# Optimization experiments

Measured on AMD Instinct MI355X. Metric: run time of the kernel, lower is better.

The kernel has to match this reference:

```python
import jax, jax.numpy as jnp
import numpy as np

D_MODEL = 1024
NUM_HEADS = 16
D_K = D_MODEL // NUM_HEADS
THETA = 10000.0
BATCH, SEQ = 2, 2048


def _rope(xh, pos):
    # xh: (..., h, s, d_k), pos: (s,) int
    half = D_K // 2
    inv_freq = THETA ** (-jnp.arange(half, dtype=jnp.float32) * 2.0 / D_K)  # (half,)
    ang = pos.astype(jnp.float32)[:, None] * inv_freq[None, :]              # (s, half)
    cos, sin = jnp.cos(ang), jnp.sin(ang)
    x1 = xh[..., 0::2]  # (..., h, s, half)
    x2 = xh[..., 1::2]
    r1 = x1 * cos - x2 * sin
    r2 = x1 * sin + x2 * cos
    out = jnp.stack([r1, r2], axis=-1)            # (..., h, s, half, 2)
    return out.reshape(xh.shape)


def setup_inputs() -> dict:
    key = jax.random.key(0)
    k1, k2, k3 = jax.random.split(key, 3)
    scale_qkv = (6.0 / (3 * D_MODEL + D_MODEL)) ** 0.5  # xavier uniform bound
    scale_o = (6.0 / (2 * D_MODEL)) ** 0.5
    return {
        "x": jax.random.normal(k1, (BATCH, SEQ, D_MODEL), dtype=jnp.float32),
        "token_positions": jnp.arange(SEQ, dtype=jnp.int64 if jax.config.jax_enable_x64 else jnp.int32),
        "qkv_proj": jax.random.uniform(k2, (3 * D_MODEL, D_MODEL), jnp.float32, -scale_qkv, scale_qkv),
        "o_proj": jax.random.uniform(k3, (D_MODEL, D_MODEL), jnp.float32, -scale_o, scale_o),
    }


def reference(x, token_positions, qkv_proj, o_proj):
    # fused QKV projection: x @ qkv_proj^T
    qkv = jnp.einsum('bsd,ed->bse', x, qkv_proj)          # (b, s, 3*d_model)
    q, k, v = jnp.split(qkv, 3, axis=-1)

    def to_heads(t):
        b, s, _ = t.shape
        return t.reshape(b, s, NUM_HEADS, D_K).transpose(0, 2, 1, 3)  # (b, h, s, d_k)

    qh, kh, vh = to_heads(q), to_heads(k), to_heads(v)
    qh = _rope(qh, token_positions)
    kh = _rope(kh, token_positions)

    scores = jnp.einsum('bhqd,bhkd->bhqk', qh, kh) / (D_K ** 0.5)
    s = x.shape[-2]
    causal = jnp.tril(jnp.ones((s, s), dtype=bool))
    scores = jnp.where(causal, scores, -jnp.inf)
    attn = jax.nn.softmax(scores, axis=-1)
    out = jnp.einsum('bhqk,bhkd->bhqd', attn, vh)          # (b, h, s, d_k)
    out = out.transpose(0, 2, 1, 3).reshape(x.shape[0], s, D_MODEL)
    return jnp.einsum('bsd,od->bso', out, o_proj)
```

## Files before the change

### kernel.cpp

```cpp
#include <hip/hip_runtime.h>
#include <hip/hip_bf16.h>
#include <math.h>

typedef __bf16 bf16_t;
typedef __attribute__((ext_vector_type(2))) __bf16 bf16x2;
typedef __attribute__((ext_vector_type(4))) __bf16 bf16x4;
typedef __attribute__((ext_vector_type(8))) __bf16 bf16x8;
typedef __attribute__((ext_vector_type(4))) float f32x4;

#define BATCH  2
#define SEQ    2048
#define DMODEL 1024
#define NHEADS 16
#define DK     64

typedef const __attribute__((address_space(1))) void* gas_t;
typedef __attribute__((address_space(3))) void* las_t;

#define X_N (BATCH * SEQ * DMODEL)
#define W_N (3 * DMODEL * DMODEL)
#define O_N (DMODEL * DMODEL)

__global__ __launch_bounds__(256) void convert_kernel(
    const float* __restrict__ x, const float* __restrict__ w, const float* __restrict__ o,
    bf16_t* __restrict__ xb, bf16_t* __restrict__ wb, bf16_t* __restrict__ ob)
{
    const int gid = blockIdx.x * 256 + threadIdx.x;
    const float* src; bf16_t* dst; int base = gid * 8;
    if (base < X_N)                { src = x; dst = xb; }
    else if (base < X_N + W_N)     { src = w; dst = wb; base -= X_N; }
    else                           { src = o; dst = ob; base -= X_N + W_N; }
    const f32x4 lo = *(const f32x4*)(src + base);
    const f32x4 hi = *(const f32x4*)(src + base + 4);
    bf16x8 r;
    r[0] = (bf16_t)lo[0]; r[1] = (bf16_t)lo[1]; r[2] = (bf16_t)lo[2]; r[3] = (bf16_t)lo[3];
    r[4] = (bf16_t)hi[0]; r[5] = (bf16_t)hi[1]; r[6] = (bf16_t)hi[2]; r[7] = (bf16_t)hi[3];
    *(bf16x8*)(dst + base) = r;
}

__device__ __forceinline__ void gemm128_body(
    const bf16_t* __restrict__ A, const bf16_t* __restrict__ B,
    int rowBase, int colBase, bf16_t* ldsA, bf16_t* ldsB, f32x4 acc[4][4])
{
    const int tid  = threadIdx.x;
    const int lane = tid & 63;
    const int l15  = lane & 15, quad = lane >> 4;
    const int qr   = ((tid >> 6) >> 1) * 64;
    const int qc   = ((tid >> 6) & 1) * 64;

    const int c0 = tid, c1 = tid + 256;
    const int r0 = c0 >> 2, kc0 = (c0 & 3) * 8;
    const int r1 = c1 >> 2, kc1 = (c1 & 3) * 8;
    const bf16_t* ga0 = A + (size_t)(rowBase + r0) * DMODEL + kc0;
    const bf16_t* ga1 = A + (size_t)(rowBase + r1) * DMODEL + kc1;
    const bf16_t* gb0 = B + (size_t)(colBase + r0) * DMODEL + kc0;
    const bf16_t* gb1 = B + (size_t)(colBase + r1) * DMODEL + kc1;

    for (int k0 = 0; k0 < DMODEL; k0 += 32) {
        __syncthreads();
        __builtin_amdgcn_global_load_lds((gas_t)(ga0 + k0), (las_t)(ldsA + c0 * 8), 16, 0, 0);
        __builtin_amdgcn_global_load_lds((gas_t)(ga1 + k0), (las_t)(ldsA + c1 * 8), 16, 0, 0);
        __builtin_amdgcn_global_load_lds((gas_t)(gb0 + k0), (las_t)(ldsB + c0 * 8), 16, 0, 0);
        __builtin_amdgcn_global_load_lds((gas_t)(gb1 + k0), (las_t)(ldsB + c1 * 8), 16, 0, 0);
        __syncthreads();

        bf16x8 af[4], bfr[4];
#pragma unroll
        for (int i = 0; i < 4; ++i)
            af[i] = *(const bf16x8*)&ldsA[(qr + i * 16 + l15) * 32 + quad * 8];
#pragma unroll
        for (int j = 0; j < 4; ++j)
            bfr[j] = *(const bf16x8*)&ldsB[(qc + j * 16 + l15) * 32 + quad * 8];
#pragma unroll
        for (int i = 0; i < 4; ++i)
#pragma unroll
            for (int j = 0; j < 4; ++j)
                acc[i][j] = __builtin_amdgcn_mfma_f32_16x16x32_bf16(af[i], bfr[j], acc[i][j], 0, 0, 0);
    }
}

__global__ __launch_bounds__(256) void qkv_gemm_kernel(
    const bf16_t* __restrict__ x, const bf16_t* __restrict__ w,
    const int* __restrict__ pos,
    bf16_t* __restrict__ qo, bf16_t* __restrict__ ko, bf16_t* __restrict__ vt)
{
    __shared__ bf16_t ldsA[128 * 32];
    __shared__ bf16_t ldsB[128 * 32];
    const int rowBase = blockIdx.y * 128;
    const int colBase = blockIdx.x * 128;
    f32x4 acc[4][4] = {};
    gemm128_body(x, w, rowBase, colBase, ldsA, ldsB, acc);

    const int lane = threadIdx.x & 63;
    const int l15 = lane & 15, quad = lane >> 4;
    const int qr = ((threadIdx.x >> 6) >> 1) * 64;
    const int qc = ((threadIdx.x >> 6) & 1) * 64;
#pragma unroll
    for (int j = 0; j < 4; ++j) {
        const int col  = colBase + qc + j * 16 + l15;
        const int part = col >> 10;
        const int h    = (col & 1023) >> 6;
        const int d    = col & 63;
        bf16_t* op = (part == 0) ? qo : (part == 1) ? ko : vt;
        if (part < 2) {
            const float invf  = exp2f(-(float)(d >> 1) * 0.4152410118609203f);
            const float psign = (d & 1) ? 1.f : -1.f;
#pragma unroll
            for (int i = 0; i < 4; ++i) {
#pragma unroll
                for (int r = 0; r < 4; ++r) {
                    const int m = rowBase + qr + i * 16 + quad * 4 + r;
                    const int b = m >> 11;
                    const int s = m & (SEQ - 1);
                    const float ang = (float)pos[s] * invf;
                    const float sn_ = __sinf(ang);
                    const float c_  = __cosf(ang);
                    const float v = acc[i][j][r];
                    const float p = __shfl_xor(v, 1);
                    const float res = fmaf(p, psign * sn_, v * c_);
                    op[((size_t)(b * NHEADS + h) * SEQ + s) * DK + d] = (bf16_t)res;
                }
            }
        } else {
#pragma unroll
            for (int i = 0; i < 4; ++i) {
#pragma unroll
                for (int r = 0; r < 4; ++r) {
                    const int m = rowBase + qr + i * 16 + quad * 4 + r;
                    const int b = m >> 11;
                    const int s = m & (SEQ - 1);
                    const int sp = (s & ~63) | ((s & 15) << 2) | ((s >> 4) & 3);
                    op[(size_t)(b * NHEADS + h) * SEQ * DK + (size_t)d * SEQ + sp]
                        = (bf16_t)acc[i][j][r];
                }
            }
        }
    }
}

__global__ __launch_bounds__(256) void out_gemm_kernel(
    const bf16_t* __restrict__ a, const bf16_t* __restrict__ w, float* __restrict__ out)
{
    __shared__ bf16_t ldsA[128 * 32];
    __shared__ bf16_t ldsB[64 * 32];
    const int tid  = threadIdx.x;
    const int lane = tid & 63;
    const int l15  = lane & 15, quad = lane >> 4;
    const int wv   = tid >> 6;
    const int rowBase = blockIdx.y * 128;
    const int colBase = blockIdx.x * 64;

    const int c0 = tid, c1 = tid + 256;
    const bf16_t* ga0 = a + (size_t)(rowBase + (c0 >> 2)) * DMODEL + (c0 & 3) * 8;
    const bf16_t* ga1 = a + (size_t)(rowBase + (c1 >> 2)) * DMODEL + (c1 & 3) * 8;
    const bf16_t* gb0 = w + (size_t)(colBase + (tid >> 2)) * DMODEL + (tid & 3) * 8;

    f32x4 acc[2][4] = {};
    for (int k0 = 0; k0 < DMODEL; k0 += 32) {
        __syncthreads();
        __builtin_amdgcn_global_load_lds((gas_t)(ga0 + k0), (las_t)(ldsA + c0 * 8), 16, 0, 0);
        __builtin_amdgcn_global_load_lds((gas_t)(ga1 + k0), (las_t)(ldsA + c1 * 8), 16, 0, 0);
        __builtin_amdgcn_global_load_lds((gas_t)(gb0 + k0), (las_t)(ldsB + tid * 8), 16, 0, 0);
        __syncthreads();

        bf16x8 af[2], bfr[4];
#pragma unroll
        for (int i = 0; i < 2; ++i)
            af[i] = *(const bf16x8*)&ldsA[(wv * 32 + i * 16 + l15) * 32 + quad * 8];
#pragma unroll
        for (int j = 0; j < 4; ++j)
            bfr[j] = *(const bf16x8*)&ldsB[(j * 16 + l15) * 32 + quad * 8];
#pragma unroll
        for (int i = 0; i < 2; ++i)
#pragma unroll
            for (int j = 0; j < 4; ++j)
                acc[i][j] = __builtin_amdgcn_mfma_f32_16x16x32_bf16(af[i], bfr[j], acc[i][j], 0, 0, 0);
    }
#pragma unroll
    for (int i = 0; i < 2; ++i) {
#pragma unroll
        for (int r = 0; r < 4; ++r) {
            const int m = rowBase + wv * 32 + i * 16 + quad * 4 + r;
#pragma unroll
            for (int j = 0; j < 4; ++j)
                out[(size_t)m * DMODEL + colBase + j * 16 + l15] = acc[i][j][r];
        }
    }
}

__global__ __launch_bounds__(512) void attn_kernel(
    const bf16_t* __restrict__ Q, const bf16_t* __restrict__ K,
    const bf16_t* __restrict__ VT, bf16_t* __restrict__ AO)
{
    __shared__ bf16_t Kb[2][64 * 64];
    __shared__ bf16_t Vb[2][64 * 64];
    __shared__ bf16_t Pb[8][16 * 72];

    const int bh = blockIdx.x & 31;
    const int j  = blockIdx.x >> 5;
    const int qb = (j < 8) ? j : 23 - j;
    const int nt = 2 * qb + 2;

    const int tid  = threadIdx.x;
    const int wave = tid >> 6, lane = tid & 63;
    const int l15  = lane & 15, quad = lane >> 4;
    const int q0   = qb * 128 + wave * 16;
    const size_t hb = (size_t)bh * SEQ * DK;

    const int sr = tid >> 3;
    const int sc = ((tid & 7) ^ (sr & 7)) * 8;
    const int dd = tid * 8;

    bf16x8 aq0, aq1;
    {
        const bf16_t* qrow = Q + hb + (size_t)(q0 + l15) * DK + quad * 8;
        aq0 = *(const bf16x8*)qrow;
        aq1 = *(const bf16x8*)(qrow + 32);
#pragma unroll
        for (int i = 0; i < 8; ++i) {
            aq0[i] = (bf16_t)((float)aq0[i] * 0.125f);
            aq1[i] = (bf16_t)((float)aq1[i] * 0.125f);
        }
    }

    f32x4 oacc[4] = {};
    float lsum[4] = {};

    __builtin_amdgcn_global_load_lds((gas_t)(K  + hb + (size_t)sr * DK + sc),
                                     (las_t)(&Kb[0][dd]), 16, 0, 0);
    __builtin_amdgcn_global_load_lds((gas_t)(VT + hb + (size_t)sr * SEQ + sc),
                                     (las_t)(&Vb[0][dd]), 16, 0, 0);
    __syncthreads();

    const int swA = (quad ^ (l15 & 7)) * 8;
    const int swB = ((4 + quad) ^ (l15 & 7)) * 8;

    int buf = 0;
    for (int kb = 0; kb < nt; ++kb) {
        if (kb + 1 < nt) {
            const bf16_t* kg = K  + hb + (size_t)(kb + 1) * 64 * DK;
            const bf16_t* vg = VT + hb + (kb + 1) * 64;
            __builtin_amdgcn_global_load_lds((gas_t)(kg + (size_t)sr * DK + sc),
                                             (las_t)(&Kb[buf ^ 1][dd]), 16, 0, 0);
            __builtin_amdgcn_global_load_lds((gas_t)(vg + (size_t)sr * SEQ + sc),
                                             (las_t)(&Vb[buf ^ 1][dd]), 16, 0, 0);
        }

        const bool act = (kb * 64 <= q0 + 15);
        const bool nm  = (kb * 64 + 63 > q0);

        if (act) {
            bf16x8 kf0[4], kf1[4];
#pragma unroll
            for (int c = 0; c < 4; ++c) {
                kf0[c] = *(const bf16x8*)&Kb[buf][(c * 16 + l15) * 64 + swA];
                kf1[c] = *(const bf16x8*)&Kb[buf][(c * 16 + l15) * 64 + swB];
            }
            f32x4 sc4[4];
#pragma unroll
            for (int c = 0; c < 4; ++c) {
                f32x4 z = {};
                z = __builtin_amdgcn_mfma_f32_16x16x32_bf16(aq0, kf0[c], z, 0, 0, 0);
                z = __builtin_amdgcn_mfma_f32_16x16x32_bf16(aq1, kf1[c], z, 0, 0, 0);
                sc4[c] = z;
            }
#pragma unroll
            for (int r = 0; r < 4; ++r) {
                bf16x4 pr;
#pragma unroll
                for (int c = 0; c < 4; ++c) {
                    float s = sc4[c][r];
                    if (nm) {
                        const int key = kb * 64 + c * 16 + l15;
                        const int qa  = q0 + quad * 4 + r;
                        s = (key <= qa) ? s : -INFINITY;
                    }
                    const float p = __expf(s - 8.0f);
                    lsum[r] += p;
                    pr[c] = (bf16_t)p;
                }
                *(bf16x4*)&Pb[wave][(quad * 4 + r) * 72 + l15 * 4] = pr;
            }
            asm volatile("s_waitcnt lgkmcnt(0)" ::: "memory");

            const bf16x8 ap0 = *(const bf16x8*)&Pb[wave][l15 * 72 + quad * 8];
            const bf16x8 ap1 = *(const bf16x8*)&Pb[wave][l15 * 72 + 32 + quad * 8];
#pragma unroll
            for (int t = 0; t < 4; ++t) {
                const bf16x8 bv0 = *(const bf16x8*)&Vb[buf][(t * 16 + l15) * 64 + swA];
                const bf16x8 bv1 = *(const bf16x8*)&Vb[buf][(t * 16 + l15) * 64 + swB];
                oacc[t] = __builtin_amdgcn_mfma_f32_16x16x32_bf16(ap0, bv0, oacc[t], 0, 0, 0);
                oacc[t] = __builtin_amdgcn_mfma_f32_16x16x32_bf16(ap1, bv1, oacc[t], 0, 0, 0);
            }
        }

        __syncthreads();
        buf ^= 1;
    }

    const int b = bh >> 4, h = bh & 15;
    float inv[4];
#pragma unroll
    for (int r = 0; r < 4; ++r) {
        float s = lsum[r];
        s += __shfl_xor(s, 1);
        s += __shfl_xor(s, 2);
        s += __shfl_xor(s, 4);
        s += __shfl_xor(s, 8);
        inv[r] = 1.0f / s;
    }
#pragma unroll
    for (int t = 0; t < 4; ++t)
#pragma unroll
        for (int r = 0; r < 4; ++r) {
            const int qa = q0 + quad * 4 + r;
            AO[(size_t)(b * SEQ + qa) * DMODEL + h * 64 + t * 16 + l15] =
                (bf16_t)(oacc[t][r] * inv[r]);
        }
}

extern "C" void kernel_launch(void* const* d_in, const int* in_sizes, int n_in,
                              void* d_out, int out_size, void* d_ws, size_t ws_size,
                              hipStream_t stream) {
    (void)in_sizes; (void)n_in; (void)out_size; (void)ws_size;
    const float* x    = (const float*)d_in[0];
    const int*   pos  = (const int*)d_in[1];
    const float* qkvw = (const float*)d_in[2];
    const float* ow   = (const float*)d_in[3];
    float* out = (float*)d_out;

    const size_t HEAD_ELEMS = (size_t)BATCH * NHEADS * SEQ * DK;
    bf16_t* Qw  = (bf16_t*)d_ws;
    bf16_t* Kw  = Qw + HEAD_ELEMS;
    bf16_t* Vt  = Kw + HEAD_ELEMS;
    bf16_t* AO  = Vt + HEAD_ELEMS;
    bf16_t* xb  = AO;
    bf16_t* wb  = AO + X_N;
    bf16_t* ob  = wb + W_N;

    convert_kernel<<<dim3(4096), 256, 0, stream>>>(x, qkvw, ow, xb, wb, ob);
    qkv_gemm_kernel<<<dim3(24, 32), 256, 0, stream>>>(xb, wb, pos, Qw, Kw, Vt);
    attn_kernel<<<dim3(512), 512, 0, stream>>>(Qw, Kw, Vt, AO);
    out_gemm_kernel<<<dim3(16, 32), 256, 0, stream>>>(AO, ob, out);
}
```

Measured before the change: 193.8 us.

## Double GEMM K-tile to 64 with XOR-swizzled LDS and precompute RoPE table

Both projection GEMMs now stage 64-wide K tiles in LDS instead of 32, which halves the number of barrier pairs per output tile. The LDS rows use an XOR swizzle on 16-byte chunks to avoid bank conflicts on the wider rows. The RoPE cos/sin values are computed once per (position, frequency) pair by extra blocks in the convert kernel and stored in a workspace table, so the QKV epilogue no longer evaluates sin/cos per element. The cost is double the LDS footprint, which may reduce occupancy, plus extra global reads of the table in the epilogue.

```diff
diff --git a/kernel.cpp b/kernel.cpp
--- a/kernel.cpp
+++ b/kernel.cpp
@@ -7,6 +7,7 @@
 typedef __attribute__((ext_vector_type(4))) __bf16 bf16x4;
 typedef __attribute__((ext_vector_type(8))) __bf16 bf16x8;
 typedef __attribute__((ext_vector_type(4))) float f32x4;
+typedef __attribute__((ext_vector_type(2))) float f32x2;
 
 #define BATCH  2
 #define SEQ    2048
@@ -20,11 +21,22 @@
 #define X_N (BATCH * SEQ * DMODEL)
 #define W_N (3 * DMODEL * DMODEL)
 #define O_N (DMODEL * DMODEL)
+#define TBL_N (SEQ * 32)
 
 __global__ __launch_bounds__(256) void convert_kernel(
     const float* __restrict__ x, const float* __restrict__ w, const float* __restrict__ o,
-    bf16_t* __restrict__ xb, bf16_t* __restrict__ wb, bf16_t* __restrict__ ob)
-{
+    const int* __restrict__ pos,
+    bf16_t* __restrict__ xb, bf16_t* __restrict__ wb, bf16_t* __restrict__ ob,
+    f32x2* __restrict__ tbl)
+{
+    if (blockIdx.x >= 4096) {
+        const int e  = (blockIdx.x - 4096) * 256 + threadIdx.x;
+        const int s  = e >> 5;
+        const int dp = e & 31;
+        const float ang = (float)pos[s] * exp2f(-(float)dp * 0.4152410118609203f);
+        tbl[e] = (f32x2){ __cosf(ang), __sinf(ang) };
+        return;
+    }
     const int gid = blockIdx.x * 256 + threadIdx.x;
     const float* src; bf16_t* dst; int base = gid * 8;
     if (base < X_N)                { src = x; dst = xb; }
@@ -45,47 +57,53 @@
     const int tid  = threadIdx.x;
     const int lane = tid & 63;
     const int l15  = lane & 15, quad = lane >> 4;
+    const int l7   = l15 & 7;
     const int qr   = ((tid >> 6) >> 1) * 64;
     const int qc   = ((tid >> 6) & 1) * 64;
 
-    const int c0 = tid, c1 = tid + 256;
-    const int r0 = c0 >> 2, kc0 = (c0 & 3) * 8;
-    const int r1 = c1 >> 2, kc1 = (c1 & 3) * 8;
-    const bf16_t* ga0 = A + (size_t)(rowBase + r0) * DMODEL + kc0;
-    const bf16_t* ga1 = A + (size_t)(rowBase + r1) * DMODEL + kc1;
-    const bf16_t* gb0 = B + (size_t)(colBase + r0) * DMODEL + kc0;
-    const bf16_t* gb1 = B + (size_t)(colBase + r1) * DMODEL + kc1;
-
-    for (int k0 = 0; k0 < DMODEL; k0 += 32) {
-        __syncthreads();
-        __builtin_amdgcn_global_load_lds((gas_t)(ga0 + k0), (las_t)(ldsA + c0 * 8), 16, 0, 0);
-        __builtin_amdgcn_global_load_lds((gas_t)(ga1 + k0), (las_t)(ldsA + c1 * 8), 16, 0, 0);
-        __builtin_amdgcn_global_load_lds((gas_t)(gb0 + k0), (las_t)(ldsB + c0 * 8), 16, 0, 0);
-        __builtin_amdgcn_global_load_lds((gas_t)(gb1 + k0), (las_t)(ldsB + c1 * 8), 16, 0, 0);
-        __syncthreads();
-
-        bf16x8 af[4], bfr[4];
-#pragma unroll
-        for (int i = 0; i < 4; ++i)
-            af[i] = *(const bf16x8*)&ldsA[(qr + i * 16 + l15) * 32 + quad * 8];
-#pragma unroll
-        for (int j = 0; j < 4; ++j)
-            bfr[j] = *(const bf16x8*)&ldsB[(qc + j * 16 + l15) * 32 + quad * 8];
-#pragma unroll
-        for (int i = 0; i < 4; ++i)
+    const int sr   = tid >> 3;
+    const int scol = ((tid & 7) ^ (sr & 7)) * 8;
+    const bf16_t* ga = A + (size_t)(rowBase + sr) * DMODEL + scol;
+    const bf16_t* gb = B + (size_t)(colBase + sr) * DMODEL + scol;
+    const int dd = tid * 8;
+
+    for (int k0 = 0; k0 < DMODEL; k0 += 64) {
+        __syncthreads();
+#pragma unroll
+        for (int u = 0; u < 4; ++u) {
+            __builtin_amdgcn_global_load_lds((gas_t)(ga + k0 + (size_t)u * 32 * DMODEL),
+                                             (las_t)(ldsA + dd + u * 2048), 16, 0, 0);
+            __builtin_amdgcn_global_load_lds((gas_t)(gb + k0 + (size_t)u * 32 * DMODEL),
+                                             (las_t)(ldsB + dd + u * 2048), 16, 0, 0);
+        }
+        __syncthreads();
+
+#pragma unroll
+        for (int kk = 0; kk < 2; ++kk) {
+            const int sw = ((kk * 4 + quad) ^ l7) * 8;
+            bf16x8 af[4], bfr[4];
+#pragma unroll
+            for (int i = 0; i < 4; ++i)
+                af[i] = *(const bf16x8*)&ldsA[(qr + i * 16 + l15) * 64 + sw];
 #pragma unroll
             for (int j = 0; j < 4; ++j)
-                acc[i][j] = __builtin_amdgcn_mfma_f32_16x16x32_bf16(af[i], bfr[j], acc[i][j], 0, 0, 0);
+                bfr[j] = *(const bf16x8*)&ldsB[(qc + j * 16 + l15) * 64 + sw];
+#pragma unroll
+            for (int i = 0; i < 4; ++i)
+#pragma unroll
+                for (int j = 0; j < 4; ++j)
+                    acc[i][j] = __builtin_amdgcn_mfma_f32_16x16x32_bf16(af[i], bfr[j], acc[i][j], 0, 0, 0);
+        }
     }
 }
 
 __global__ __launch_bounds__(256) void qkv_gemm_kernel(
     const bf16_t* __restrict__ x, const bf16_t* __restrict__ w,
-    const int* __restrict__ pos,
+    const f32x2* __restrict__ tbl,
     bf16_t* __restrict__ qo, bf16_t* __restrict__ ko, bf16_t* __restrict__ vt)
 {
-    __shared__ bf16_t ldsA[128 * 32];
-    __shared__ bf16_t ldsB[128 * 32];
+    __shared__ bf16_t ldsA[128 * 64];
+    __shared__ bf16_t ldsB[128 * 64];
     const int rowBase = blockIdx.y * 128;
     const int colBase = blockIdx.x * 128;
     f32x4 acc[4][4] = {};
@@ -103,8 +121,8 @@
         const int d    = col & 63;
         bf16_t* op = (part == 0) ? qo : (part == 1) ? ko : vt;
         if (part < 2) {
-            const float invf  = exp2f(-(float)(d >> 1) * 0.4152410118609203f);
             const float psign = (d & 1) ? 1.f : -1.f;
+            const f32x2* trow = tbl + (d >> 1);
 #pragma unroll
             for (int i = 0; i < 4; ++i) {
 #pragma unroll
@@ -112,12 +130,10 @@
                     const int m = rowBase + qr + i * 16 + quad * 4 + r;
                     const int b = m >> 11;
                     const int s = m & (SEQ - 1);
-                    const float ang = (float)pos[s] * invf;
-                    const float sn_ = __sinf(ang);
-                    const float c_  = __cosf(ang);
+                    const f32x2 cs = trow[s * 32];
                     const float v = acc[i][j][r];
                     const float p = __shfl_xor(v, 1);
-                    const float res = fmaf(p, psign * sn_, v * c_);
+                    const float res = fmaf(p, psign * cs[1], v * cs[0]);
                     op[((size_t)(b * NHEADS + h) * SEQ + s) * DK + d] = (bf16_t)res;
                 }
             }
@@ -141,40 +157,51 @@
 __global__ __launch_bounds__(256) void out_gemm_kernel(
     const bf16_t* __restrict__ a, const bf16_t* __restrict__ w, float* __restrict__ out)
 {
-    __shared__ bf16_t ldsA[128 * 32];
-    __shared__ bf16_t ldsB[64 * 32];
+    __shared__ bf16_t ldsA[128 * 64];
+    __shared__ bf16_t ldsB[64 * 64];
     const int tid  = threadIdx.x;
     const int lane = tid & 63;
     const int l15  = lane & 15, quad = lane >> 4;
+    const int l7   = l15 & 7;
     const int wv   = tid >> 6;
     const int rowBase = blockIdx.y * 128;
     const int colBase = blockIdx.x * 64;
 
-    const int c0 = tid, c1 = tid + 256;
-    const bf16_t* ga0 = a + (size_t)(rowBase + (c0 >> 2)) * DMODEL + (c0 & 3) * 8;
-    const bf16_t* ga1 = a + (size_t)(rowBase + (c1 >> 2)) * DMODEL + (c1 & 3) * 8;
-    const bf16_t* gb0 = w + (size_t)(colBase + (tid >> 2)) * DMODEL + (tid & 3) * 8;
+    const int sr   = tid >> 3;
+    const int scol = ((tid & 7) ^ (sr & 7)) * 8;
+    const bf16_t* ga = a + (size_t)(rowBase + sr) * DMODEL + scol;
+    const bf16_t* gb = w + (size_t)(colBase + sr) * DMODEL + scol;
+    const int dd = tid * 8;
 
     f32x4 acc[2][4] = {};
-    for (int k0 = 0; k0 < DMODEL; k0 += 32) {
-        __syncthreads();
-        __builtin_amdgcn_global_load_lds((gas_t)(ga0 + k0), (las_t)(ldsA + c0 * 8), 16, 0, 0);
-        __builtin_amdgcn_global_load_lds((gas_t)(ga1 + k0), (las_t)(ldsA + c1 * 8), 16, 0, 0);
-        __builtin_amdgcn_global_load_lds((gas_t)(gb0 + k0), (las_t)(ldsB + tid * 8), 16, 0, 0);
-        __syncthreads();
-
-        bf16x8 af[2], bfr[4];
-#pragma unroll
-        for (int i = 0; i < 2; ++i)
-            af[i] = *(const bf16x8*)&ldsA[(wv * 32 + i * 16 + l15) * 32 + quad * 8];
-#pragma unroll
-        for (int j = 0; j < 4; ++j)
-            bfr[j] = *(const bf16x8*)&ldsB[(j * 16 + l15) * 32 + quad * 8];
-#pragma unroll
-        for (int i = 0; i < 2; ++i)
+    for (int k0 = 0; k0 < DMODEL; k0 += 64) {
+        __syncthreads();
+#pragma unroll
+        for (int u = 0; u < 4; ++u)
+            __builtin_amdgcn_global_load_lds((gas_t)(ga + k0 + (size_t)u * 32 * DMODEL),
+                                             (las_t)(ldsA + dd + u * 2048), 16, 0, 0);
+#pragma unroll
+        for (int u = 0; u < 2; ++u)
+            __builtin_amdgcn_global_load_lds((gas_t)(gb + k0 + (size_t)u * 32 * DMODEL),
+                                             (las_t)(ldsB + dd + u * 2048), 16, 0, 0);
+        __syncthreads();
+
+#pragma unroll
+        for (int kk = 0; kk < 2; ++kk) {
+            const int sw = ((kk * 4 + quad) ^ l7) * 8;
+            bf16x8 af[2], bfr[4];
+#pragma unroll
+            for (int i = 0; i < 2; ++i)
+                af[i] = *(const bf16x8*)&ldsA[(wv * 32 + i * 16 + l15) * 64 + sw];
 #pragma unroll
             for (int j = 0; j < 4; ++j)
-                acc[i][j] = __builtin_amdgcn_mfma_f32_16x16x32_bf16(af[i], bfr[j], acc[i][j], 0, 0, 0);
+                bfr[j] = *(const bf16x8*)&ldsB[(j * 16 + l15) * 64 + sw];
+#pragma unroll
+            for (int i = 0; i < 2; ++i)
+#pragma unroll
+                for (int j = 0; j < 4; ++j)
+                    acc[i][j] = __builtin_amdgcn_mfma_f32_16x16x32_bf16(af[i], bfr[j], acc[i][j], 0, 0, 0);
+        }
     }
 #pragma unroll
     for (int i = 0; i < 2; ++i) {
@@ -337,9 +364,10 @@
     bf16_t* xb  = AO;
     bf16_t* wb  = AO + X_N;
     bf16_t* ob  = wb + W_N;
-
-    convert_kernel<<<dim3(4096), 256, 0, stream>>>(x, qkvw, ow, xb, wb, ob);
-    qkv_gemm_kernel<<<dim3(24, 32), 256, 0, stream>>>(xb, wb, pos, Qw, Kw, Vt);
+    f32x2*  tbl = (f32x2*)(ob + O_N);
+
+    convert_kernel<<<dim3(4096 + 256), 256, 0, stream>>>(x, qkvw, ow, pos, xb, wb, ob, tbl);
+    qkv_gemm_kernel<<<dim3(24, 32), 256, 0, stream>>>(xb, wb, tbl, Qw, Kw, Vt);
     attn_kernel<<<dim3(512), 512, 0, stream>>>(Qw, Kw, Vt, AO);
     out_gemm_kernel<<<dim3(16, 32), 256, 0, stream>>>(AO, ob, out);
 }
```

Measured after the change: 184.5 us. 4.8% less time.

## Double-buffer out-projection GEMM with BK=64 and XOR-swizzled LDS layout

Applied to the files above, without the earlier changes.

The output-projection GEMM now uses two LDS buffers, prefetching the next 64-wide K slice while MFMAs run on the current one. The K step doubles from 32 to 64, and a XOR swizzle on the column chunk index is meant to avoid LDS bank conflicts on fragment reads. Together these halve the barriers per K and hide global load latency, at the cost of four times the LDS per block, which may reduce occupancy.

```diff
diff --git a/kernel.cpp b/kernel.cpp
--- a/kernel.cpp
+++ b/kernel.cpp
@@ -141,40 +141,66 @@
 __global__ __launch_bounds__(256) void out_gemm_kernel(
     const bf16_t* __restrict__ a, const bf16_t* __restrict__ w, float* __restrict__ out)
 {
-    __shared__ bf16_t ldsA[128 * 32];
-    __shared__ bf16_t ldsB[64 * 32];
+    __shared__ bf16_t ldsA[2 * 128 * 64];
+    __shared__ bf16_t ldsB[2 * 64 * 64];
     const int tid  = threadIdx.x;
     const int lane = tid & 63;
     const int l15  = lane & 15, quad = lane >> 4;
+    const int l7   = l15 & 7;
     const int wv   = tid >> 6;
     const int rowBase = blockIdx.y * 128;
     const int colBase = blockIdx.x * 64;
 
-    const int c0 = tid, c1 = tid + 256;
-    const bf16_t* ga0 = a + (size_t)(rowBase + (c0 >> 2)) * DMODEL + (c0 & 3) * 8;
-    const bf16_t* ga1 = a + (size_t)(rowBase + (c1 >> 2)) * DMODEL + (c1 & 3) * 8;
-    const bf16_t* gb0 = w + (size_t)(colBase + (tid >> 2)) * DMODEL + (tid & 3) * 8;
+    const int sr   = tid >> 3;
+    const int scol = ((tid & 7) ^ (sr & 7)) * 8;
+    const bf16_t* ga = a + (size_t)(rowBase + sr) * DMODEL + scol;
+    const bf16_t* gb = w + (size_t)(colBase + sr) * DMODEL + scol;
+    const int dd = tid * 8;
+
+#pragma unroll
+    for (int u = 0; u < 4; ++u)
+        __builtin_amdgcn_global_load_lds((gas_t)(ga + (size_t)u * 32 * DMODEL),
+                                         (las_t)(ldsA + dd + u * 2048), 16, 0, 0);
+#pragma unroll
+    for (int u = 0; u < 2; ++u)
+        __builtin_amdgcn_global_load_lds((gas_t)(gb + (size_t)u * 32 * DMODEL),
+                                         (las_t)(ldsB + dd + u * 2048), 16, 0, 0);
+    __syncthreads();
 
     f32x4 acc[2][4] = {};
-    for (int k0 = 0; k0 < DMODEL; k0 += 32) {
+    int buf = 0;
+    for (int k0 = 0; k0 < DMODEL; k0 += 64) {
+        if (k0 + 64 < DMODEL) {
+            const int offA = (buf ^ 1) * 8192, offB = (buf ^ 1) * 4096;
+#pragma unroll
+            for (int u = 0; u < 4; ++u)
+                __builtin_amdgcn_global_load_lds((gas_t)(ga + k0 + 64 + (size_t)u * 32 * DMODEL),
+                                                 (las_t)(ldsA + offA + dd + u * 2048), 16, 0, 0);
+#pragma unroll
+            for (int u = 0; u < 2; ++u)
+                __builtin_amdgcn_global_load_lds((gas_t)(gb + k0 + 64 + (size_t)u * 32 * DMODEL),
+                                                 (las_t)(ldsB + offB + dd + u * 2048), 16, 0, 0);
+        }
+        const bf16_t* La = ldsA + buf * 8192;
+        const bf16_t* Lb = ldsB + buf * 4096;
+#pragma unroll
+        for (int kk = 0; kk < 2; ++kk) {
+            const int sw = ((kk * 4 + quad) ^ l7) * 8;
+            bf16x8 af[2], bfr[4];
+#pragma unroll
+            for (int i = 0; i < 2; ++i)
+                af[i] = *(const bf16x8*)&La[(wv * 32 + i * 16 + l15) * 64 + sw];
+#pragma unroll
+            for (int j = 0; j < 4; ++j)
+                bfr[j] = *(const bf16x8*)&Lb[(j * 16 + l15) * 64 + sw];
+#pragma unroll
+            for (int i = 0; i < 2; ++i)
+#pragma unroll
+                for (int j = 0; j < 4; ++j)
+                    acc[i][j] = __builtin_amdgcn_mfma_f32_16x16x32_bf16(af[i], bfr[j], acc[i][j], 0, 0, 0);
+        }
         __syncthreads();
-        __builtin_amdgcn_global_load_lds((gas_t)(ga0 + k0), (las_t)(ldsA + c0 * 8), 16, 0, 0);
-        __builtin_amdgcn_global_load_lds((gas_t)(ga1 + k0), (las_t)(ldsA + c1 * 8), 16, 0, 0);
-        __builtin_amdgcn_global_load_lds((gas_t)(gb0 + k0), (las_t)(ldsB + tid * 8), 16, 0, 0);
-        __syncthreads();
-
-        bf16x8 af[2], bfr[4];
-#pragma unroll
-        for (int i = 0; i < 2; ++i)
-            af[i] = *(const bf16x8*)&ldsA[(wv * 32 + i * 16 + l15) * 32 + quad * 8];
-#pragma unroll
-        for (int j = 0; j < 4; ++j)
-            bfr[j] = *(const bf16x8*)&ldsB[(j * 16 + l15) * 32 + quad * 8];
-#pragma unroll
-        for (int i = 0; i < 2; ++i)
-#pragma unroll
-            for (int j = 0; j < 4; ++j)
-                acc[i][j] = __builtin_amdgcn_mfma_f32_16x16x32_bf16(af[i], bfr[j], acc[i][j], 0, 0, 0);
+        buf ^= 1;
     }
 #pragma unroll
     for (int i = 0; i < 2; ++i) {
```

Result: no change. 190.8 us (-1.6%).
